# Kernel tuning notes

Hardware: AMD Instinct MI355X
Metric: run time of the kernel (lower is better)

## Reference

```python
import jax, jax.numpy as jnp
import numpy as np
from jax import lax

B, HB, WB, CB = 128, 64, 64, 16      # board batch, height, width, channels
HI, WI, CI = 72, 72, 4               # image size/channels (fixed by module)
HIDC = CB - 4                         # board hidden channels = 12
IMGC = 72                             # img_channel_n
POSTC = IMGC + 4                      # 76
FIRE_RATE = 0.5
BN_EPS = 1e-3                         # keras BatchNormalization default epsilon


def setup_inputs() -> dict:
    key = jax.random.key(0)
    k = jax.random.split(key, 8)
    x = jax.random.normal(k[0], (B, HB, WB, CB), jnp.float32)
    images = jax.random.uniform(k[1], (B, HI, WI, CI), jnp.float32)
    conv1_w = jax.random.normal(k[2], (3, 3, CI, 32), jnp.float32) * (1.0 / np.sqrt(9 * CI))
    conv2_w = jax.random.normal(k[3], (3, 3, 32, 32), jnp.float32) * (1.0 / np.sqrt(9 * 32))
    flat = (HI // 4) * (WI // 4) * 32  # 18*18*32 = 10368 after two 2x2 pools
    dense_w = jax.random.normal(k[4], (flat, HIDC * IMGC), jnp.float32) * (1.0 / np.sqrt(flat))
    upd_w1 = jax.random.normal(k[5], (POSTC * 3, 128), jnp.float32) * (1.0 / np.sqrt(POSTC * 3))
    upd_w2 = jax.random.normal(k[6], (128, CB), jnp.float32) * 0.02
    return dict(
        x=x, images=images,
        bn1_gamma=jnp.ones((CI,), jnp.float32), bn1_beta=jnp.zeros((CI,), jnp.float32),
        bn1_mean=jnp.zeros((CI,), jnp.float32), bn1_var=jnp.ones((CI,), jnp.float32),
        conv1_w=conv1_w, conv1_b=jnp.zeros((32,), jnp.float32),
        bn2_gamma=jnp.ones((32,), jnp.float32), bn2_beta=jnp.zeros((32,), jnp.float32),
        bn2_mean=jnp.zeros((32,), jnp.float32), bn2_var=jnp.ones((32,), jnp.float32),
        conv2_w=conv2_w, conv2_b=jnp.zeros((32,), jnp.float32),
        dense_w=dense_w, dense_b=jnp.zeros((HIDC * IMGC,), jnp.float32),
        upd_w1=upd_w1, upd_b1=jnp.zeros((128,), jnp.float32),
        upd_w2=upd_w2, upd_b2=jnp.zeros((CB,), jnp.float32),
    )


def _bn(x, g, b, m, v):
    return (x - m) * lax.rsqrt(v + BN_EPS) * g + b


def _conv_same(x, w, b):
    return lax.conv_general_dilated(x, w, (1, 1), 'SAME',
                                    dimension_numbers=('NHWC', 'HWIO', 'NHWC')) + b


def _maxpool2(x):
    return lax.reduce_window(x, -jnp.inf, lax.max, (1, 2, 2, 1), (1, 2, 2, 1), 'VALID')


def _living_mask(x):
    alpha = x[..., 3:4]
    return lax.reduce_window(alpha, -jnp.inf, lax.max, (1, 3, 3, 1), (1, 1, 1, 1), 'SAME') > 0.1


def _perception_kernel(c):
    # identity + sobel-x + sobel-y, depthwise with multiplier 3 (channel-major order c*3+m)
    ident = np.zeros((3, 3), np.float32); ident[1, 1] = 1.0
    sx = (np.outer([1, 2, 1], [-1, 0, 1]) / 8.0).astype(np.float32)
    sy = sx.T
    k = np.stack([ident, sx, sy], -1)       # (3,3,3)
    k = np.tile(k, (1, 1, c))                # (3,3,3c)
    return jnp.asarray(k[:, :, None, :])     # HWIO with I=1, O=3c


def reference(x, images, bn1_gamma, bn1_beta, bn1_mean, bn1_var, conv1_w, conv1_b,
              bn2_gamma, bn2_beta, bn2_mean, bn2_var, conv2_w, conv2_b,
              dense_w, dense_b, upd_w1, upd_b1, upd_w2, upd_b2):
    # ---- image model (inference mode: BN uses moving stats, dropout = identity) ----
    h = _bn(images, bn1_gamma, bn1_beta, bn1_mean, bn1_var)
    h = jax.nn.relu(_conv_same(h, conv1_w, conv1_b))
    h = _maxpool2(h)
    h = _bn(h, bn2_gamma, bn2_beta, bn2_mean, bn2_var)
    h = jax.nn.relu(_conv_same(h, conv2_w, conv2_b))
    h = _maxpool2(h)
    h = h.reshape(h.shape[0], -1)
    h = jax.nn.relu(h @ dense_w + dense_b)
    filters = h.reshape(-1, HIDC, IMGC)      # (B, 12, 72): per-sample 1x1 conv filter

    # ---- CA step ----
    pre_life = _living_mask(x)
    board_out = x[..., :4]
    hidden = x[..., 4:]
    # per-batch 1x1 VALID conv == batched channel contraction
    img_conv = jnp.einsum('bhwc,bco->bhwo', hidden, filters)
    img_aware = jnp.concatenate([board_out, img_conv], axis=-1)   # (B,H,W,76)
    kern = _perception_kernel(POSTC)
    perceived = lax.conv_general_dilated(img_aware, kern, (1, 1), 'SAME',
                                         dimension_numbers=('NHWC', 'HWIO', 'NHWC'),
                                         feature_group_count=POSTC)  # (B,H,W,228)
    u = jax.nn.relu(jnp.einsum('bhwc,cd->bhwd', perceived, upd_w1) + upd_b1)
    dx = jnp.einsum('bhwd,de->bhwe', u, upd_w2) + upd_b2
    update_mask = jax.random.uniform(jax.random.key(42), x[..., :1].shape) <= FIRE_RATE
    x = x + dx * update_mask.astype(x.dtype)
    post_life = _living_mask(x)
    living = (pre_life & post_life).astype(x.dtype)
    return x * living
```

## Files before the change

kernel.cpp:

```cpp
#include <hip/hip_runtime.h>

#define BN_EPS 1e-3f

typedef __attribute__((ext_vector_type(8))) short bf16x8;
typedef __attribute__((ext_vector_type(4))) short s16x4;
typedef __attribute__((ext_vector_type(4))) float f32x4;
typedef __attribute__((ext_vector_type(4))) unsigned u32x4;

__device__ __forceinline__ unsigned short f2bf_rne(float f) {
  unsigned u = __float_as_uint(f);
  unsigned r = u + 0x7fffu + ((u >> 16) & 1u);
  return (unsigned short)(r >> 16);
}
__device__ __forceinline__ float bf2f(unsigned short h) {
  return __uint_as_float(((unsigned)h) << 16);
}
__device__ __forceinline__ void split2(float v, unsigned short& h, unsigned short& l) {
  h = f2bf_rne(v);
  l = f2bf_rne(v - bf2f(h));
}
__device__ __forceinline__ void split2t(float v, unsigned short& h, unsigned short& l) {
  unsigned u = __float_as_uint(v);
  float hi = __uint_as_float(u & 0xFFFF0000u);
  h = (unsigned short)(u >> 16);
  l = f2bf_rne(v - hi);
}
__device__ __forceinline__ unsigned pack_bf2(float v) {
  unsigned u = __float_as_uint(v);
  float lof = v - __uint_as_float(u & 0xFFFF0000u);
  unsigned lb = __float_as_uint(lof);
  unsigned rr = lb + 0x7fffu + ((lb >> 16) & 1u);
  return (u >> 16) | (rr & 0xFFFF0000u);
}

__device__ __forceinline__ unsigned rotl32(unsigned v, int n) {
  return (v << n) | (v >> (32 - n));
}

__device__ __forceinline__ float tf42_uniform(unsigned i) {
  unsigned x0 = 0u, x1 = i;
  const unsigned k0 = 0u, k1 = 42u, k2 = 0u ^ 42u ^ 0x1BD11BDAu;
  x0 += k0; x1 += k1;
#define TFR(r) { x0 += x1; x1 = rotl32(x1, r); x1 ^= x0; }
  TFR(13) TFR(15) TFR(26) TFR(6)
  x0 += k1; x1 += k2 + 1u;
  TFR(17) TFR(29) TFR(16) TFR(24)
  x0 += k2; x1 += k0 + 2u;
  TFR(13) TFR(15) TFR(26) TFR(6)
  x0 += k0; x1 += k1 + 3u;
  TFR(17) TFR(29) TFR(16) TFR(24)
  x0 += k1; x1 += k2 + 4u;
  TFR(13) TFR(15) TFR(26) TFR(6)
  x0 += k2; x1 += k0 + 5u;
#undef TFR
  unsigned bits = x0 ^ x1;
  return __uint_as_float((bits >> 9) | 0x3F800000u) - 1.0f;
}

__global__ __launch_bounds__(256) void k_prep_w(
    const float* __restrict__ w1, const float* __restrict__ w2,
    const float* __restrict__ W2d,
    unsigned short* __restrict__ W1h, unsigned short* __restrict__ W1l,
    unsigned short* __restrict__ W2h_, unsigned short* __restrict__ W2l_,
    unsigned short* __restrict__ WD2h, unsigned short* __restrict__ WD2l) {
  int blk = blockIdx.x, tid = threadIdx.x;
  if (blk < 12) {
    int t = blk * 256 + tid;
    int j = t & 7, l = (t >> 3) & 63, nt = (t >> 9) & 1, ks = t >> 10;
    int k = 32 * ks + ((l >> 4) << 3) + j;
    int tap = k >> 3, ci = k & 7;
    float v = (tap < 9 && ci < 4) ? w1[tap * 128 + ci * 32 + nt * 16 + (l & 15)] : 0.f;
    unsigned short hh, ll; split2(v, hh, ll);
    W1h[t] = hh; W1l[t] = ll;
  } else if (blk < 48) {
    int t = (blk - 12) * 256 + tid;
    int j = t & 7, l = (t >> 3) & 63, nt = (t >> 9) & 1, tap = t >> 10;
    int ci = ((l >> 4) << 3) + j, co = nt * 16 + (l & 15);
    float v = w2[tap * 1024 + ci * 32 + co];
    unsigned short hh, ll; split2(v, hh, ll);
    W2h_[t] = hh; W2l_[t] = ll;
  } else {
    for (int t = tid; t < 2048; t += 256) {
      int j = t & 7, l = (t >> 3) & 63, ks = t >> 9;
      int k = 32 * ks + ((l >> 4) << 3) + j;
      int col = l & 15;
      float v = W2d[k * 16 + col];
      unsigned short hh, ll; split2(v, hh, ll);
      WD2h[t] = hh; WD2l[t] = ll;
    }
  }
}

__global__ __launch_bounds__(256) void k_conv1(
    const float* __restrict__ img,
    const float* __restrict__ g1, const float* __restrict__ be1,
    const float* __restrict__ m1, const float* __restrict__ v1,
    const unsigned short* __restrict__ Wc1h, const unsigned short* __restrict__ Wc1l,
    const float* __restrict__ bias,
    const float* __restrict__ g2, const float* __restrict__ be2,
    const float* __restrict__ m2, const float* __restrict__ v2,
    float* __restrict__ h1) {
  __shared__ __align__(16) unsigned short Lh[2592];
  __shared__ __align__(16) unsigned short Ll[2592];
  int tid = threadIdx.x;
  int b = blockIdx.y;
  int tY = (blockIdx.x / 5) * 16, tX = (blockIdx.x % 5) * 16;
  float s1[4], t1[4];
#pragma unroll
  for (int ci = 0; ci < 4; ++ci) {
    float s = g1[ci] / sqrtf(v1[ci] + BN_EPS);
    s1[ci] = s; t1[ci] = be1[ci] - m1[ci] * s;
  }
  const s16x4 z4 = {0, 0, 0, 0};
  for (int idx = tid; idx < 324; idx += 256) {
    int ly = idx / 18, lx = idx - ly * 18;
    int gy = tY - 1 + ly, gx = tX - 1 + lx;
    float4 v = {0.f, 0.f, 0.f, 0.f};
    if (gy >= 0 && gy < 72 && gx >= 0 && gx < 72) {
      v = *(const float4*)(img + (((size_t)b * 72 + gy) * 72 + gx) * 4);
      v.x = v.x * s1[0] + t1[0];
      v.y = v.y * s1[1] + t1[1];
      v.z = v.z * s1[2] + t1[2];
      v.w = v.w * s1[3] + t1[3];
    }
    unsigned short ha, la, hb, lb, hc, lc, hd, ld;
    split2t(v.x, ha, la); split2t(v.y, hb, lb);
    split2t(v.z, hc, lc); split2t(v.w, hd, ld);
    s16x4 vh = {(short)ha, (short)hb, (short)hc, (short)hd};
    s16x4 vl = {(short)la, (short)lb, (short)lc, (short)ld};
    *(s16x4*)(Lh + idx * 8) = vh;
    *(s16x4*)(Lh + idx * 8 + 4) = z4;
    *(s16x4*)(Ll + idx * 8) = vl;
    *(s16x4*)(Ll + idx * 8 + 4) = z4;
  }
  __syncthreads();
  int wv = tid >> 6, lane = tid & 63;
  int lr = lane & 15, lhi = lane >> 4;
  int nt = wv & 1, mrow0 = (wv >> 1) * 8;
  bf16x8 wh[3], wl[3];
#pragma unroll
  for (int ks = 0; ks < 3; ++ks) {
    int base = ((ks * 2 + nt) * 64 + lane) * 8;
    wh[ks] = *(const bf16x8*)(Wc1h + base);
    wl[ks] = *(const bf16x8*)(Wc1l + base);
  }
  f32x4 acc[8];
#pragma unroll
  for (int mt = 0; mt < 8; ++mt) acc[mt] = (f32x4){0.f, 0.f, 0.f, 0.f};
#pragma unroll
  for (int ks = 0; ks < 3; ++ks) {
    int tap = 4 * ks + lhi;
    int tc = tap > 8 ? 8 : tap;
    int dy = tc / 3, dx = tc - 3 * dy;
#pragma unroll
    for (int mt = 0; mt < 8; ++mt) {
      int row = mrow0 + mt;
      int px = (row + dy) * 18 + lr + dx;
      bf16x8 ah = *(const bf16x8*)(Lh + px * 8);
      bf16x8 al = *(const bf16x8*)(Ll + px * 8);
      acc[mt] = __builtin_amdgcn_mfma_f32_16x16x32_bf16(ah, wh[ks], acc[mt], 0, 0, 0);
      acc[mt] = __builtin_amdgcn_mfma_f32_16x16x32_bf16(ah, wl[ks], acc[mt], 0, 0, 0);
      acc[mt] = __builtin_amdgcn_mfma_f32_16x16x32_bf16(al, wh[ks], acc[mt], 0, 0, 0);
    }
  }
  int co = nt * 16 + lr;
  float bv = bias[co];
  float s2 = g2[co] / sqrtf(v2[co] + BN_EPS);
  float t2 = be2[co] - m2[co] * s2;
#pragma unroll
  for (int a = 0; a < 4; ++a) {
#pragma unroll
    for (int bb = 0; bb < 2; ++bb) {
      float v00 = fmaxf(acc[2 * a][2 * bb] + bv, 0.f);
      float v01 = fmaxf(acc[2 * a][2 * bb + 1] + bv, 0.f);
      float v10 = fmaxf(acc[2 * a + 1][2 * bb] + bv, 0.f);
      float v11 = fmaxf(acc[2 * a + 1][2 * bb + 1] + bv, 0.f);
      float p = fmaxf(fmaxf(v00, v01), fmaxf(v10, v11));
      int gy = (tY >> 1) + (mrow0 >> 1) + a;
      int gx = (tX >> 1) + lhi * 2 + bb;
      if (gy < 36 && gx < 36)
        h1[(((size_t)b * 36 + gy) * 36 + gx) * 32 + co] = p * s2 + t2;
    }
  }
}

__global__ __launch_bounds__(256, 3) void k_conv2(
    const float* __restrict__ hin,
    const unsigned short* __restrict__ Wch, const unsigned short* __restrict__ Wcl,
    const float* __restrict__ bias, float* __restrict__ h2) {
  __shared__ __align__(16) unsigned short Lh[12960];
  __shared__ __align__(16) unsigned short Ll[12960];
  int tid = threadIdx.x;
  int b = blockIdx.y;
  int tY = (blockIdx.x / 3) * 16, tX = (blockIdx.x % 3) * 16;
  for (int idx = tid; idx < 2592; idx += 256) {
    int pix = idx >> 3, c4 = idx & 7;
    int ly = pix / 18, lx = pix - ly * 18;
    int gy = tY - 1 + ly, gx = tX - 1 + lx;
    float4 v = {0.f, 0.f, 0.f, 0.f};
    if (gy >= 0 && gy < 36 && gx >= 0 && gx < 36)
      v = *(const float4*)(hin + (((size_t)b * 36 + gy) * 36 + gx) * 32 + c4 * 4);
    unsigned short ha, la, hb, lb, hc, lc, hd, ld;
    split2t(v.x, ha, la); split2t(v.y, hb, lb);
    split2t(v.z, hc, lc); split2t(v.w, hd, ld);
    s16x4 vh = {(short)ha, (short)hb, (short)hc, (short)hd};
    s16x4 vl = {(short)la, (short)lb, (short)lc, (short)ld};
    *(s16x4*)(Lh + pix * 40 + c4 * 4) = vh;
    *(s16x4*)(Ll + pix * 40 + c4 * 4) = vl;
  }
  __syncthreads();
  int wv = tid >> 6, lane = tid & 63;
  int lr = lane & 15, lhi = lane >> 4;
  int nt = wv & 1, mrow0 = (wv >> 1) * 8;
  bf16x8 wh[9], wl[9];
#pragma unroll
  for (int tap = 0; tap < 9; ++tap) {
    int base = ((tap * 2 + nt) * 64 + lane) * 8;
    wh[tap] = *(const bf16x8*)(Wch + base);
    wl[tap] = *(const bf16x8*)(Wcl + base);
  }
  f32x4 acc[8];
#pragma unroll
  for (int mt = 0; mt < 8; ++mt) acc[mt] = (f32x4){0.f, 0.f, 0.f, 0.f};
#pragma unroll
  for (int mt = 0; mt < 8; ++mt) {
    int row = mrow0 + mt;
#pragma unroll
    for (int tap = 0; tap < 9; ++tap) {
      int dy = tap / 3, dx = tap - dy * 3;
      int pixel = (row + dy) * 18 + (lr + dx);
      bf16x8 ah = *(const bf16x8*)(Lh + pixel * 40 + lhi * 8);
      bf16x8 al = *(const bf16x8*)(Ll + pixel * 40 + lhi * 8);
      acc[mt] = __builtin_amdgcn_mfma_f32_16x16x32_bf16(ah, wh[tap], acc[mt], 0, 0, 0);
      acc[mt] = __builtin_amdgcn_mfma_f32_16x16x32_bf16(ah, wl[tap], acc[mt], 0, 0, 0);
      acc[mt] = __builtin_amdgcn_mfma_f32_16x16x32_bf16(al, wh[tap], acc[mt], 0, 0, 0);
    }
  }
  int co = nt * 16 + lr;
  float bv = bias[co];
#pragma unroll
  for (int a = 0; a < 4; ++a) {
#pragma unroll
    for (int bb = 0; bb < 2; ++bb) {
      float v00 = fmaxf(acc[2 * a][2 * bb] + bv, 0.f);
      float v01 = fmaxf(acc[2 * a][2 * bb + 1] + bv, 0.f);
      float v10 = fmaxf(acc[2 * a + 1][2 * bb] + bv, 0.f);
      float v11 = fmaxf(acc[2 * a + 1][2 * bb + 1] + bv, 0.f);
      float p = fmaxf(fmaxf(v00, v01), fmaxf(v10, v11));
      int gy = (tY >> 1) + (mrow0 >> 1) + a;
      int gx = (tX >> 1) + lhi * 2 + bb;
      if (gy < 18 && gx < 18)
        h2[(((size_t)b * 18 + gy) * 18 + gx) * 32 + co] = p;
    }
  }
}

__global__ __launch_bounds__(256) void k_dense_part(
    const float* __restrict__ h2, const float* __restrict__ w,
    float* __restrict__ part) {
  __shared__ __align__(16) unsigned short Ah[128 * 40];
  __shared__ __align__(16) unsigned short Al[128 * 40];
  __shared__ __align__(16) unsigned short Bh[64 * 40];
  __shared__ __align__(16) unsigned short Bl[64 * 40];
  int tid = threadIdx.x;
  int n0 = blockIdx.x * 64;
  int kc = blockIdx.y;
  int wv = tid >> 6, lane = tid & 63;
  int lr = lane & 15, lhi = lane >> 4;
  f32x4 acc[8];
#pragma unroll
  for (int m = 0; m < 8; ++m) acc[m] = (f32x4){0.f, 0.f, 0.f, 0.f};
  for (int kt = 0; kt < 18; ++kt) {
    int kb = kc * 576 + kt * 32;
    if (kt) __syncthreads();
#pragma unroll
    for (int it = 0; it < 4; ++it) {
      int f = tid + it * 256;
      int ml = f >> 3, kq = f & 7;
      float4 p = *(const float4*)(h2 + (size_t)ml * 10368 + kb + kq * 4);
      unsigned short h0, l0, h1, l1, h2_, l2_, h3, l3;
      split2t(p.x, h0, l0); split2t(p.y, h1, l1);
      split2t(p.z, h2_, l2_); split2t(p.w, h3, l3);
      s16x4 vh = {(short)h0, (short)h1, (short)h2_, (short)h3};
      s16x4 vl = {(short)l0, (short)l1, (short)l2_, (short)l3};
      *(s16x4*)(Ah + ml * 40 + kq * 4) = vh;
      *(s16x4*)(Al + ml * 40 + kq * 4) = vl;
    }
#pragma unroll
    for (int it = 0; it < 2; ++it) {
      int f = tid + it * 256;
      int kr = f >> 4, n4 = (f & 15) * 4;
      float4 p = {0.f, 0.f, 0.f, 0.f};
      if (n0 + n4 < 864)
        p = *(const float4*)(w + (size_t)(kb + kr) * 864 + n0 + n4);
      unsigned short hh, ll;
      split2t(p.x, hh, ll); Bh[(n4 + 0) * 40 + kr] = hh; Bl[(n4 + 0) * 40 + kr] = ll;
      split2t(p.y, hh, ll); Bh[(n4 + 1) * 40 + kr] = hh; Bl[(n4 + 1) * 40 + kr] = ll;
      split2t(p.z, hh, ll); Bh[(n4 + 2) * 40 + kr] = hh; Bl[(n4 + 2) * 40 + kr] = ll;
      split2t(p.w, hh, ll); Bh[(n4 + 3) * 40 + kr] = hh; Bl[(n4 + 3) * 40 + kr] = ll;
    }
    __syncthreads();
    bf16x8 bh_ = *(const bf16x8*)(Bh + (wv * 16 + lr) * 40 + lhi * 8);
    bf16x8 bl_ = *(const bf16x8*)(Bl + (wv * 16 + lr) * 40 + lhi * 8);
#pragma unroll
    for (int m = 0; m < 8; ++m) {
      bf16x8 ah = *(const bf16x8*)(Ah + (m * 16 + lr) * 40 + lhi * 8);
      bf16x8 al = *(const bf16x8*)(Al + (m * 16 + lr) * 40 + lhi * 8);
      acc[m] = __builtin_amdgcn_mfma_f32_16x16x32_bf16(ah, bh_, acc[m], 0, 0, 0);
      acc[m] = __builtin_amdgcn_mfma_f32_16x16x32_bf16(ah, bl_, acc[m], 0, 0, 0);
      acc[m] = __builtin_amdgcn_mfma_f32_16x16x32_bf16(al, bh_, acc[m], 0, 0, 0);
    }
  }
  int n = n0 + wv * 16 + lr;
  if (n < 864) {
#pragma unroll
    for (int m = 0; m < 8; ++m) {
#pragma unroll
      for (int r = 0; r < 4; ++r) {
        int mm = m * 16 + lhi * 4 + r;
        part[((size_t)kc * 128 + mm) * 864 + n] = acc[m][r];
      }
    }
  }
}

__global__ __launch_bounds__(256) void k_finprep(
    const float* __restrict__ part, const float* __restrict__ bias,
    const float* __restrict__ W1,
    unsigned short* __restrict__ Eh, unsigned short* __restrict__ El) {
  __shared__ float fl[864];
  int b = blockIdx.x;
  int tid = threadIdx.x;
  for (int e = tid; e < 864; e += 256) {
    float s = bias[e];
#pragma unroll
    for (int kc = 0; kc < 18; ++kc) s += part[(size_t)kc * 110592 + b * 864 + e];
    fl[e] = fmaxf(s, 0.f);
  }
  __syncthreads();
  int col = tid & 127;
  int k0 = tid >> 7;
  for (int k = k0; k < 64; k += 2) {
    float v;
    if (k < 12) {
      v = W1[k * 128 + col];
    } else if (k < 48) {
      int h = (k - 12) / 3, t = (k - 12) % 3;
      const float* wp = W1 + (12 + t) * 128 + col;
      const float* fp = fl + h * 72;
      float a0 = 0.f, a1 = 0.f, a2 = 0.f, a3 = 0.f;
      for (int c = 0; c < 72; c += 4) {
        a0 = fmaf(fp[c], wp[(size_t)c * 384], a0);
        a1 = fmaf(fp[c + 1], wp[(size_t)(c + 1) * 384], a1);
        a2 = fmaf(fp[c + 2], wp[(size_t)(c + 2) * 384], a2);
        a3 = fmaf(fp[c + 3], wp[(size_t)(c + 3) * 384], a3);
      }
      v = (a0 + a1) + (a2 + a3);
    } else {
      v = 0.f;
    }
    unsigned short hh, ll;
    split2(v, hh, ll);
    int ks = k >> 5, j = k & 7, a4 = (k >> 3) & 3;
    int l = a4 * 16 + (col & 15), nt = col >> 4;
    size_t o = (((size_t)b * 8 + nt) * 2 + ks) * 512 + l * 8 + j;
    Eh[o] = hh;
    El[o] = ll;
  }
}

__global__ __launch_bounds__(256, 4) void k_ca(
    const float* __restrict__ x,
    const unsigned short* __restrict__ Eh, const unsigned short* __restrict__ El,
    const float* __restrict__ B1,
    const unsigned short* __restrict__ W2h, const unsigned short* __restrict__ W2l,
    const float* __restrict__ B2,
    float* __restrict__ xnew, float* __restrict__ aold,
    float* __restrict__ anew) {
  __shared__ __align__(16) unsigned char S[34048];
  float* ia = (float*)S;
  unsigned short* PAh = (unsigned short*)(S + 7680);
  unsigned short* PAl = (unsigned short*)(S + 16896);
  unsigned* U32 = (unsigned*)S;
  float* mskL = (float*)(S + 33792);

  int tid = threadIdx.x;
  int b = blockIdx.y;
  int tx = (blockIdx.x & 7) * 8, ty = (blockIdx.x >> 3) * 8;
  int wv = tid >> 6, lane = tid & 63;
  int lr = lane & 15, lhi = lane >> 4;

  bf16x8 bh[2][2], bl[2][2];
#pragma unroll
  for (int nt = 0; nt < 2; ++nt)
#pragma unroll
    for (int ks = 0; ks < 2; ++ks) {
      size_t base = (((size_t)b * 8 + (wv * 2 + nt)) * 2 + ks) * 512 + lane * 8;
      bh[nt][ks] = *(const bf16x8*)(Eh + base);
      bl[nt][ks] = *(const bf16x8*)(El + base);
    }
  float xo[4];
#pragma unroll
  for (int r = 0; r < 4; ++r) {
    int px = wv * 16 + lhi * 4 + r;
    int gy = ty + (px >> 3), gx = tx + (px & 7);
    xo[r] = x[(((size_t)b * 64 + gy) * 64 + gx) * 16 + lr];
  }

  if (tid < 200) {
    int px_ = tid >> 1, half = tid & 1;
    int hy = px_ / 10, hx = px_ - hy * 10;
    int pp = hy * 12 + hx;
    int gy = ty + hy - 1, gx = tx + hx - 1;
    float4 v0 = {0.f, 0.f, 0.f, 0.f}, v1 = {0.f, 0.f, 0.f, 0.f};
    if (gy >= 0 && gy < 64 && gx >= 0 && gx < 64) {
      const float* xp = x + (((size_t)b * 64 + gy) * 64 + gx) * 16 + half * 8;
      v0 = *(const float4*)xp;
      v1 = *(const float4*)(xp + 4);
    }
    int c0 = half * 8;
    ia[(c0 + 0) * 120 + pp] = v0.x; ia[(c0 + 1) * 120 + pp] = v0.y;
    ia[(c0 + 2) * 120 + pp] = v0.z; ia[(c0 + 3) * 120 + pp] = v0.w;
    ia[(c0 + 4) * 120 + pp] = v1.x; ia[(c0 + 5) * 120 + pp] = v1.y;
    ia[(c0 + 6) * 120 + pp] = v1.z; ia[(c0 + 7) * 120 + pp] = v1.w;
  }
  {
    if (tid >= 192) {
      int p = tid - 192;
      int gy = ty + (p >> 3), gx = tx + (p & 7);
      unsigned pix = (unsigned)(b * 4096 + gy * 64 + gx);
      mskL[p] = (tf42_uniform(pix) <= 0.5f) ? 1.f : 0.f;
    }
    const s16x4 z4 = {0, 0, 0, 0};
    if (wv == 2) {
#pragma unroll
      for (int g = 0; g < 4; ++g) *(s16x4*)(PAh + lane * 72 + 48 + 4 * g) = z4;
    }
    if (wv == 3) {
#pragma unroll
      for (int g = 0; g < 4; ++g) *(s16x4*)(PAl + lane * 72 + 48 + 4 * g) = z4;
    }
  }
  __syncthreads();

  {
    int py = lane >> 3, pxx = lane & 7;
    const float* pc0 = ia + (py + 1) * 12 + (pxx + 1);
    unsigned short oh[12], ol[12];
#pragma unroll
    for (int i = 0; i < 4; ++i) {
      const float* pc = pc0 + (wv * 4 + i) * 120;
      float n00 = pc[-13], n01 = pc[-12], n02 = pc[-11];
      float n10 = pc[-1],  n11 = pc[0],   n12 = pc[1];
      float n20 = pc[11],  n21 = pc[12],  n22 = pc[13];
      float pid = n11;
      float psx = ((n02 - n00) + 2.f * (n12 - n10) + (n22 - n20)) * 0.125f;
      float psy = ((n20 - n00) + 2.f * (n21 - n01) + (n22 - n02)) * 0.125f;
      split2t(pid, oh[3 * i + 0], ol[3 * i + 0]);
      split2t(psx, oh[3 * i + 1], ol[3 * i + 1]);
      split2t(psy, oh[3 * i + 2], ol[3 * i + 2]);
    }
    int off = lane * 72 + wv * 12;
#pragma unroll
    for (int g = 0; g < 3; ++g) {
      s16x4 vh = {(short)oh[4 * g], (short)oh[4 * g + 1],
                  (short)oh[4 * g + 2], (short)oh[4 * g + 3]};
      s16x4 vl = {(short)ol[4 * g], (short)ol[4 * g + 1],
                  (short)ol[4 * g + 2], (short)ol[4 * g + 3]};
      *(s16x4*)(PAh + off + 4 * g) = vh;
      *(s16x4*)(PAl + off + 4 * g) = vl;
    }
  }
  __syncthreads();

  f32x4 acc[4][2];
#pragma unroll
  for (int m = 0; m < 4; ++m)
#pragma unroll
    for (int nt = 0; nt < 2; ++nt)
      acc[m][nt] = (f32x4){0.f, 0.f, 0.f, 0.f};
#pragma unroll
  for (int ks = 0; ks < 2; ++ks) {
#pragma unroll
    for (int m = 0; m < 4; ++m) {
      int arow = m * 16 + lr;
      bf16x8 pah = *(const bf16x8*)(PAh + arow * 72 + ks * 32 + lhi * 8);
      bf16x8 pal = *(const bf16x8*)(PAl + arow * 72 + ks * 32 + lhi * 8);
#pragma unroll
      for (int nt = 0; nt < 2; ++nt) {
        acc[m][nt] = __builtin_amdgcn_mfma_f32_16x16x32_bf16(
            pah, bh[nt][ks], acc[m][nt], 0, 0, 0);
        acc[m][nt] = __builtin_amdgcn_mfma_f32_16x16x32_bf16(
            pah, bl[nt][ks], acc[m][nt], 0, 0, 0);
        acc[m][nt] = __builtin_amdgcn_mfma_f32_16x16x32_bf16(
            pal, bh[nt][ks], acc[m][nt], 0, 0, 0);
      }
    }
  }
  bf16x8 ch_[4], cl_[4];
#pragma unroll
  for (int ks = 0; ks < 4; ++ks) {
    ch_[ks] = *(const bf16x8*)(W2h + ks * 512 + lane * 8);
    cl_[ks] = *(const bf16x8*)(W2l + ks * 512 + lane * 8);
  }
  __syncthreads();

  int d0 = wv * 32;
  float b1v0 = B1[d0 + lr], b1v1 = B1[d0 + 16 + lr];
#pragma unroll
  for (int m = 0; m < 4; ++m)
#pragma unroll
    for (int nt = 0; nt < 2; ++nt) {
      float bv = nt ? b1v1 : b1v0;
      int hid = d0 + nt * 16 + lr;
#pragma unroll
      for (int r = 0; r < 4; ++r) {
        int px = m * 16 + lhi * 4 + r;
        U32[px * 132 + hid] = pack_bf2(fmaxf(acc[m][nt][r] + bv, 0.f));
      }
    }
  __syncthreads();

  union Cvt { unsigned d[4]; bf16x8 v8; };
  f32x4 acc2 = {0.f, 0.f, 0.f, 0.f};
  const unsigned* urow = U32 + (wv * 16 + lr) * 132;
#pragma unroll
  for (int ks = 0; ks < 4; ++ks) {
    u32x4 q0 = *(const u32x4*)(urow + ks * 32 + lhi * 8);
    u32x4 q1 = *(const u32x4*)(urow + ks * 32 + lhi * 8 + 4);
    Cvt ah, al;
#pragma unroll
    for (int i = 0; i < 2; ++i) {
      unsigned p0 = q0[2 * i], p1 = q0[2 * i + 1];
      ah.d[i] = (p0 & 0xffffu) | (p1 << 16);
      al.d[i] = (p0 >> 16) | (p1 & 0xffff0000u);
    }
#pragma unroll
    for (int i = 0; i < 2; ++i) {
      unsigned p0 = q1[2 * i], p1 = q1[2 * i + 1];
      ah.d[2 + i] = (p0 & 0xffffu) | (p1 << 16);
      al.d[2 + i] = (p0 >> 16) | (p1 & 0xffff0000u);
    }
    acc2 = __builtin_amdgcn_mfma_f32_16x16x32_bf16(ah.v8, ch_[ks], acc2, 0, 0, 0);
    acc2 = __builtin_amdgcn_mfma_f32_16x16x32_bf16(ah.v8, cl_[ks], acc2, 0, 0, 0);
    acc2 = __builtin_amdgcn_mfma_f32_16x16x32_bf16(al.v8, ch_[ks], acc2, 0, 0, 0);
  }

  float b2v = B2[lr];
#pragma unroll
  for (int r = 0; r < 4; ++r) {
    int px = wv * 16 + lhi * 4 + r;
    int gy = ty + (px >> 3), gx = tx + (px & 7);
    float m_ = mskL[px];
    float xn = xo[r] + (acc2[r] + b2v) * m_;
    size_t o = (((size_t)b * 64 + gy) * 64 + gx) * 16 + lr;
    xnew[o] = xn;
    if (lr == 3) {
      unsigned pix = (unsigned)(b * 4096 + gy * 64 + gx);
      aold[pix] = xo[r];
      anew[pix] = xn;
    }
  }
}

__global__ __launch_bounds__(256) void k_final(
    float* __restrict__ xnew, const float* __restrict__ aold,
    const float* __restrict__ anew) {
  int t = blockIdx.x * 256 + threadIdx.x;
  int gx = t & 63, gy = (t >> 6) & 63, b = t >> 12;
  float mo = -1e30f, mn = -1e30f;
  for (int dy = -1; dy <= 1; ++dy) {
    int yy = gy + dy; if (yy < 0 || yy >= 64) continue;
    for (int dx = -1; dx <= 1; ++dx) {
      int xx = gx + dx; if (xx < 0 || xx >= 64) continue;
      int p = b * 4096 + yy * 64 + xx;
      mo = fmaxf(mo, aold[p]);
      mn = fmaxf(mn, anew[p]);
    }
  }
  float live = (mo > 0.1f && mn > 0.1f) ? 1.f : 0.f;
  size_t base = (size_t)t * 16;
#pragma unroll
  for (int c4 = 0; c4 < 4; ++c4) {
    float4 v = *(const float4*)(xnew + base + c4 * 4);
    v.x *= live; v.y *= live; v.z *= live; v.w *= live;
    *(float4*)(xnew + base + c4 * 4) = v;
  }
}

extern "C" void kernel_launch(void* const* d_in, const int* in_sizes, int n_in,
                              void* d_out, int out_size, void* d_ws, size_t ws_size,
                              hipStream_t stream) {
  const float* x    = (const float*)d_in[0];
  const float* img  = (const float*)d_in[1];
  const float* g1   = (const float*)d_in[2];
  const float* be1  = (const float*)d_in[3];
  const float* m1   = (const float*)d_in[4];
  const float* v1   = (const float*)d_in[5];
  const float* w1c  = (const float*)d_in[6];
  const float* b1c  = (const float*)d_in[7];
  const float* g2   = (const float*)d_in[8];
  const float* be2  = (const float*)d_in[9];
  const float* m2   = (const float*)d_in[10];
  const float* v2   = (const float*)d_in[11];
  const float* w2c  = (const float*)d_in[12];
  const float* b2c  = (const float*)d_in[13];
  const float* dw   = (const float*)d_in[14];
  const float* db   = (const float*)d_in[15];
  const float* uw1  = (const float*)d_in[16];
  const float* ub1  = (const float*)d_in[17];
  const float* uw2  = (const float*)d_in[18];
  const float* ub2  = (const float*)d_in[19];

  char* ws = (char*)d_ws;
  float* h1   = (float*)(ws);
  float* part = h1;
  float* h2   = (float*)(ws + 21233664);
  float* aold = (float*)(ws + 26542080);
  float* anew = (float*)(ws + 28639232);
  unsigned short* W2Bh = (unsigned short*)(ws + 30736384);
  unsigned short* W2Bl = (unsigned short*)(ws + 30740480);
  unsigned short* Wc2h = (unsigned short*)(ws + 30744576);
  unsigned short* Wc2l = (unsigned short*)(ws + 30763008);
  unsigned short* Wc1h = (unsigned short*)(ws + 30781440);
  unsigned short* Wc1l = (unsigned short*)(ws + 30787584);
  unsigned short* W1Eh = (unsigned short*)(ws + 30793728);
  unsigned short* W1El = (unsigned short*)(ws + 32890880);
  float* xnew = (float*)d_out;

  k_prep_w<<<49, 256, 0, stream>>>(w1c, w2c, uw2, Wc1h, Wc1l, Wc2h, Wc2l,
                                   W2Bh, W2Bl);
  k_conv1<<<dim3(25, 128), 256, 0, stream>>>(img, g1, be1, m1, v1, Wc1h, Wc1l,
                                             b1c, g2, be2, m2, v2, h1);
  k_conv2<<<dim3(9, 128), 256, 0, stream>>>(h1, Wc2h, Wc2l, b2c, h2);
  k_dense_part<<<dim3(14, 18), 256, 0, stream>>>(h2, dw, part);
  k_finprep<<<128, 256, 0, stream>>>(part, db, uw1, W1Eh, W1El);
  k_ca<<<dim3(64, 128), 256, 0, stream>>>(x, W1Eh, W1El, ub1, W2Bh, W2Bl, ub2,
                                          xnew, aold, anew);
  k_final<<<2048, 256, 0, stream>>>(xnew, aold, anew);
}
```

Measured before the change: 177.9 us.

## Fold perception stencil into per-sample update weights; contract raw 3x3 taps via MFMA

```diff
diff --git a/kernel.cpp b/kernel.cpp
--- a/kernel.cpp
+++ b/kernel.cpp
@@ -327,8 +327,9 @@
 __global__ __launch_bounds__(256) void k_finprep(
     const float* __restrict__ part, const float* __restrict__ bias,
     const float* __restrict__ W1,
-    unsigned short* __restrict__ Eh, unsigned short* __restrict__ El) {
+    unsigned short* __restrict__ Th, unsigned short* __restrict__ Tl) {
   __shared__ float fl[864];
+  __shared__ float W1e[48 * 128];
   int b = blockIdx.x;
   int tid = threadIdx.x;
   for (int e = tid; e < 864; e += 256) {
@@ -338,49 +339,63 @@
     fl[e] = fmaxf(s, 0.f);
   }
   __syncthreads();
-  int col = tid & 127;
-  int k0 = tid >> 7;
-  for (int k = k0; k < 64; k += 2) {
-    float v;
-    if (k < 12) {
-      v = W1[k * 128 + col];
-    } else if (k < 48) {
-      int h = (k - 12) / 3, t = (k - 12) % 3;
-      const float* wp = W1 + (12 + t) * 128 + col;
-      const float* fp = fl + h * 72;
-      float a0 = 0.f, a1 = 0.f, a2 = 0.f, a3 = 0.f;
-      for (int c = 0; c < 72; c += 4) {
-        a0 = fmaf(fp[c], wp[(size_t)c * 384], a0);
-        a1 = fmaf(fp[c + 1], wp[(size_t)(c + 1) * 384], a1);
-        a2 = fmaf(fp[c + 2], wp[(size_t)(c + 2) * 384], a2);
-        a3 = fmaf(fp[c + 3], wp[(size_t)(c + 3) * 384], a3);
+  {
+    int col = tid & 127;
+    int k0 = tid >> 7;
+    for (int k = k0; k < 48; k += 2) {
+      float v;
+      if (k < 12) {
+        v = W1[k * 128 + col];
+      } else {
+        int h = (k - 12) / 3, t = (k - 12) % 3;
+        const float* wp = W1 + (12 + t) * 128 + col;
+        const float* fp = fl + h * 72;
+        float a0 = 0.f, a1 = 0.f, a2 = 0.f, a3 = 0.f;
+        for (int c = 0; c < 72; c += 4) {
+          a0 = fmaf(fp[c], wp[(size_t)c * 384], a0);
+          a1 = fmaf(fp[c + 1], wp[(size_t)(c + 1) * 384], a1);
+          a2 = fmaf(fp[c + 2], wp[(size_t)(c + 2) * 384], a2);
+          a3 = fmaf(fp[c + 3], wp[(size_t)(c + 3) * 384], a3);
+        }
+        v = (a0 + a1) + (a2 + a3);
       }
-      v = (a0 + a1) + (a2 + a3);
-    } else {
-      v = 0.f;
+      W1e[k * 128 + col] = v;
+    }
+  }
+  __syncthreads();
+  const float kid[9] = {0.f, 0.f, 0.f, 0.f, 1.f, 0.f, 0.f, 0.f, 0.f};
+  const float ksx[9] = {-0.125f, 0.f, 0.125f, -0.25f, 0.f, 0.25f, -0.125f, 0.f, 0.125f};
+  const float ksy[9] = {-0.125f, -0.25f, -0.125f, 0.f, 0.f, 0.f, 0.125f, 0.25f, 0.125f};
+  for (int e = tid; e < 20480; e += 256) {
+    int j = e & 7, l = (e >> 3) & 63, r = e >> 9;
+    int ks = r % 5;
+    int k = 32 * ks + ((l >> 4) << 3) + j;
+    int col = 16 * (r / 5) + (l & 15);
+    float v = 0.f;
+    if (k < 144) {
+      int tap = k >> 4, c = k & 15;
+      const float* we = W1e + 3 * c * 128 + col;
+      v = kid[tap] * we[0] + ksx[tap] * we[128] + ksy[tap] * we[256];
     }
     unsigned short hh, ll;
     split2(v, hh, ll);
-    int ks = k >> 5, j = k & 7, a4 = (k >> 3) & 3;
-    int l = a4 * 16 + (col & 15), nt = col >> 4;
-    size_t o = (((size_t)b * 8 + nt) * 2 + ks) * 512 + l * 8 + j;
-    Eh[o] = hh;
-    El[o] = ll;
-  }
-}
-
-__global__ __launch_bounds__(256, 4) void k_ca(
+    size_t o = (size_t)b * 20480 + e;
+    Th[o] = hh;
+    Tl[o] = ll;
+  }
+}
+
+__global__ __launch_bounds__(256) void k_ca(
     const float* __restrict__ x,
-    const unsigned short* __restrict__ Eh, const unsigned short* __restrict__ El,
+    const unsigned short* __restrict__ Th, const unsigned short* __restrict__ Tl,
     const float* __restrict__ B1,
     const unsigned short* __restrict__ W2h, const unsigned short* __restrict__ W2l,
     const float* __restrict__ B2,
     float* __restrict__ xnew, float* __restrict__ aold,
     float* __restrict__ anew) {
   __shared__ __align__(16) unsigned char S[34048];
-  float* ia = (float*)S;
-  unsigned short* PAh = (unsigned short*)(S + 7680);
-  unsigned short* PAl = (unsigned short*)(S + 16896);
+  unsigned short* Hh = (unsigned short*)S;
+  unsigned short* Hl = (unsigned short*)(S + 4800);
   unsigned* U32 = (unsigned*)S;
   float* mskL = (float*)(S + 33792);
 
@@ -390,14 +405,14 @@
   int wv = tid >> 6, lane = tid & 63;
   int lr = lane & 15, lhi = lane >> 4;
 
-  bf16x8 bh[2][2], bl[2][2];
+  bf16x8 bh[2][5], bl[2][5];
 #pragma unroll
   for (int nt = 0; nt < 2; ++nt)
 #pragma unroll
-    for (int ks = 0; ks < 2; ++ks) {
-      size_t base = (((size_t)b * 8 + (wv * 2 + nt)) * 2 + ks) * 512 + lane * 8;
-      bh[nt][ks] = *(const bf16x8*)(Eh + base);
-      bl[nt][ks] = *(const bf16x8*)(El + base);
+    for (int ks = 0; ks < 5; ++ks) {
+      size_t base = (((size_t)b * 8 + (wv * 2 + nt)) * 5 + ks) * 512 + lane * 8;
+      bh[nt][ks] = *(const bf16x8*)(Th + base);
+      bl[nt][ks] = *(const bf16x8*)(Tl + base);
     }
   float xo[4];
 #pragma unroll
@@ -410,7 +425,6 @@
   if (tid < 200) {
     int px_ = tid >> 1, half = tid & 1;
     int hy = px_ / 10, hx = px_ - hy * 10;
-    int pp = hy * 12 + hx;
     int gy = ty + hy - 1, gx = tx + hx - 1;
     float4 v0 = {0.f, 0.f, 0.f, 0.f}, v1 = {0.f, 0.f, 0.f, 0.f};
     if (gy >= 0 && gy < 64 && gx >= 0 && gx < 64) {
@@ -418,58 +432,27 @@
       v0 = *(const float4*)xp;
       v1 = *(const float4*)(xp + 4);
     }
-    int c0 = half * 8;
-    ia[(c0 + 0) * 120 + pp] = v0.x; ia[(c0 + 1) * 120 + pp] = v0.y;
-    ia[(c0 + 2) * 120 + pp] = v0.z; ia[(c0 + 3) * 120 + pp] = v0.w;
-    ia[(c0 + 4) * 120 + pp] = v1.x; ia[(c0 + 5) * 120 + pp] = v1.y;
-    ia[(c0 + 6) * 120 + pp] = v1.z; ia[(c0 + 7) * 120 + pp] = v1.w;
-  }
-  {
-    if (tid >= 192) {
-      int p = tid - 192;
-      int gy = ty + (p >> 3), gx = tx + (p & 7);
-      unsigned pix = (unsigned)(b * 4096 + gy * 64 + gx);
-      mskL[p] = (tf42_uniform(pix) <= 0.5f) ? 1.f : 0.f;
-    }
-    const s16x4 z4 = {0, 0, 0, 0};
-    if (wv == 2) {
-#pragma unroll
-      for (int g = 0; g < 4; ++g) *(s16x4*)(PAh + lane * 72 + 48 + 4 * g) = z4;
-    }
-    if (wv == 3) {
-#pragma unroll
-      for (int g = 0; g < 4; ++g) *(s16x4*)(PAl + lane * 72 + 48 + 4 * g) = z4;
-    }
-  }
-  __syncthreads();
-
-  {
-    int py = lane >> 3, pxx = lane & 7;
-    const float* pc0 = ia + (py + 1) * 12 + (pxx + 1);
-    unsigned short oh[12], ol[12];
-#pragma unroll
-    for (int i = 0; i < 4; ++i) {
-      const float* pc = pc0 + (wv * 4 + i) * 120;
-      float n00 = pc[-13], n01 = pc[-12], n02 = pc[-11];
-      float n10 = pc[-1],  n11 = pc[0],   n12 = pc[1];
-      float n20 = pc[11],  n21 = pc[12],  n22 = pc[13];
-      float pid = n11;
-      float psx = ((n02 - n00) + 2.f * (n12 - n10) + (n22 - n20)) * 0.125f;
-      float psy = ((n20 - n00) + 2.f * (n21 - n01) + (n22 - n02)) * 0.125f;
-      split2t(pid, oh[3 * i + 0], ol[3 * i + 0]);
-      split2t(psx, oh[3 * i + 1], ol[3 * i + 1]);
-      split2t(psy, oh[3 * i + 2], ol[3 * i + 2]);
-    }
-    int off = lane * 72 + wv * 12;
-#pragma unroll
-    for (int g = 0; g < 3; ++g) {
-      s16x4 vh = {(short)oh[4 * g], (short)oh[4 * g + 1],
-                  (short)oh[4 * g + 2], (short)oh[4 * g + 3]};
-      s16x4 vl = {(short)ol[4 * g], (short)ol[4 * g + 1],
-                  (short)ol[4 * g + 2], (short)ol[4 * g + 3]};
-      *(s16x4*)(PAh + off + 4 * g) = vh;
-      *(s16x4*)(PAl + off + 4 * g) = vl;
-    }
+    unsigned short h0, l0, h1, l1, h2, l2, h3, l3;
+    unsigned short h4, l4, h5, l5, h6, l6, h7, l7;
+    split2t(v0.x, h0, l0); split2t(v0.y, h1, l1);
+    split2t(v0.z, h2, l2); split2t(v0.w, h3, l3);
+    split2t(v1.x, h4, l4); split2t(v1.y, h5, l5);
+    split2t(v1.z, h6, l6); split2t(v1.w, h7, l7);
+    s16x4 a0 = {(short)h0, (short)h1, (short)h2, (short)h3};
+    s16x4 a1 = {(short)h4, (short)h5, (short)h6, (short)h7};
+    s16x4 c0v = {(short)l0, (short)l1, (short)l2, (short)l3};
+    s16x4 c1v = {(short)l4, (short)l5, (short)l6, (short)l7};
+    int off = px_ * 24 + half * 8;
+    *(s16x4*)(Hh + off) = a0;
+    *(s16x4*)(Hh + off + 4) = a1;
+    *(s16x4*)(Hl + off) = c0v;
+    *(s16x4*)(Hl + off + 4) = c1v;
+  }
+  if (tid >= 192) {
+    int p = tid - 192;
+    int gy = ty + (p >> 3), gx = tx + (p & 7);
+    unsigned pix = (unsigned)(b * 4096 + gy * 64 + gx);
+    mskL[p] = (tf42_uniform(pix) <= 0.5f) ? 1.f : 0.f;
   }
   __syncthreads();
 
@@ -479,21 +462,26 @@
 #pragma unroll
     for (int nt = 0; nt < 2; ++nt)
       acc[m][nt] = (f32x4){0.f, 0.f, 0.f, 0.f};
-#pragma unroll
-  for (int ks = 0; ks < 2; ++ks) {
+  int c0 = (lhi & 1) * 8;
+#pragma unroll
+  for (int ks = 0; ks < 5; ++ks) {
+    int tap = 2 * ks + (lhi >> 1);
+    int tc = tap > 8 ? 8 : tap;
+    int dy = tc / 3, dx = tc - 3 * dy;
 #pragma unroll
     for (int m = 0; m < 4; ++m) {
-      int arow = m * 16 + lr;
-      bf16x8 pah = *(const bf16x8*)(PAh + arow * 72 + ks * 32 + lhi * 8);
-      bf16x8 pal = *(const bf16x8*)(PAl + arow * 72 + ks * 32 + lhi * 8);
+      int px = m * 16 + lr;
+      int hp = ((px >> 3) + dy) * 10 + (px & 7) + dx;
+      bf16x8 ah = *(const bf16x8*)(Hh + hp * 24 + c0);
+      bf16x8 al = *(const bf16x8*)(Hl + hp * 24 + c0);
 #pragma unroll
       for (int nt = 0; nt < 2; ++nt) {
         acc[m][nt] = __builtin_amdgcn_mfma_f32_16x16x32_bf16(
-            pah, bh[nt][ks], acc[m][nt], 0, 0, 0);
+            ah, bh[nt][ks], acc[m][nt], 0, 0, 0);
         acc[m][nt] = __builtin_amdgcn_mfma_f32_16x16x32_bf16(
-            pah, bl[nt][ks], acc[m][nt], 0, 0, 0);
+            ah, bl[nt][ks], acc[m][nt], 0, 0, 0);
         acc[m][nt] = __builtin_amdgcn_mfma_f32_16x16x32_bf16(
-            pal, bh[nt][ks], acc[m][nt], 0, 0, 0);
+            al, bh[nt][ks], acc[m][nt], 0, 0, 0);
       }
     }
   }
@@ -624,8 +612,8 @@
   unsigned short* Wc2l = (unsigned short*)(ws + 30763008);
   unsigned short* Wc1h = (unsigned short*)(ws + 30781440);
   unsigned short* Wc1l = (unsigned short*)(ws + 30787584);
-  unsigned short* W1Eh = (unsigned short*)(ws + 30793728);
-  unsigned short* W1El = (unsigned short*)(ws + 32890880);
+  unsigned short* Tth  = (unsigned short*)(ws + 30793728);
+  unsigned short* Ttl  = (unsigned short*)(ws + 36036608);
   float* xnew = (float*)d_out;
 
   k_prep_w<<<49, 256, 0, stream>>>(w1c, w2c, uw2, Wc1h, Wc1l, Wc2h, Wc2l,
@@ -634,8 +622,8 @@
                                              b1c, g2, be2, m2, v2, h1);
   k_conv2<<<dim3(9, 128), 256, 0, stream>>>(h1, Wc2h, Wc2l, b2c, h2);
   k_dense_part<<<dim3(14, 18), 256, 0, stream>>>(h2, dw, part);
-  k_finprep<<<128, 256, 0, stream>>>(part, db, uw1, W1Eh, W1El);
-  k_ca<<<dim3(64, 128), 256, 0, stream>>>(x, W1Eh, W1El, ub1, W2Bh, W2Bl, ub2,
+  k_finprep<<<128, 256, 0, stream>>>(part, db, uw1, Tth, Ttl);
+  k_ca<<<dim3(64, 128), 256, 0, stream>>>(x, Tth, Ttl, ub1, W2Bh, W2Bl, ub2,
                                           xnew, aold, anew);
   k_final<<<2048, 256, 0, stream>>>(xnew, aold, anew);
 }
```

New measurement: 228.7 us. +28.5%, slower.
